# Kernel optimization log

Hardware: AMD Instinct MI355X
Metric: run time of the kernel (lower is better)

The kernel has to match this reference:

```python
import jax, jax.numpy as jnp
import numpy as np

B, L, H, E = 4, 1024, 8, 64
MODES = 64
SCALE = float(1.0 / np.sqrt(512.0))        # 1/sqrt(out_channels)
N_TOP = int(5 * np.ceil(np.log(L)))        # factor * ceil(log(L_Q)) = 35


def setup_inputs() -> dict:
    key = jax.random.key(0)
    k1, k2, k3, k4, k5, k6, k7 = jax.random.split(key, 7)
    rng = np.random.default_rng(0)
    mode_index = jnp.asarray(np.sort(rng.choice(L // 2, MODES, replace=False)), dtype=jnp.int32)
    return {
        "tf_queries": jax.random.normal(k1, (B, L, H, E), dtype=jnp.float32),
        "queries": jax.random.normal(k2, (B, L, H, E), dtype=jnp.float32),
        "keys": jax.random.normal(k3, (B, L, H, E), dtype=jnp.float32),
        "values": jax.random.normal(k4, (B, L, H, E), dtype=jnp.float32),
        "weights1_real": SCALE * jax.random.uniform(k5, (H, E, E, MODES), dtype=jnp.float32),
        "weights1_imag": SCALE * jax.random.uniform(k6, (H, E, E, MODES), dtype=jnp.float32),
        "mix_weights": jax.random.uniform(k7, (H, L, 2), dtype=jnp.float32),
        "mask": jnp.ones((B, L), dtype=jnp.bool_),
        "mode_index": mode_index,
    }


def _sig_scores(q_blhe, k_blhe, corr):
    # q_blhe, k_blhe: [B, L, H, E]
    q = jnp.transpose(q_blhe, (0, 2, 1, 3))  # [B,H,L,E]
    k = jnp.transpose(k_blhe, (0, 2, 1, 3))  # [B,H,L,E]
    if corr:
        # FFT autocorrelation along time
        qf = jnp.fft.rfft(jnp.transpose(q_blhe, (0, 2, 3, 1)), axis=-1)  # [B,H,E,F]
        kf = jnp.fft.rfft(jnp.transpose(k_blhe, (0, 2, 3, 1)), axis=-1)
        ac = jnp.fft.irfft(qf * jnp.conj(kf), n=L, axis=-1)              # [B,H,E,L]
        ac = jnp.transpose(ac, (0, 1, 3, 2))                             # [B,H,L,E]
    else:
        ac = q
    amp = jnp.linalg.norm(ac, axis=-1)                # [B,H,L]
    _, top_idx = jax.lax.top_k(amp, N_TOP)            # [B,H,n]
    q_sel = jnp.take_along_axis(q, top_idx[..., None], axis=2)          # [B,H,n,E]
    scores = jnp.einsum('bhnd,bhmd->bhnm', q_sel, k) * SCALE            # [B,H,n,L]
    full = jnp.full((q.shape[0], H, L, L), -jnp.inf, dtype=q.dtype)
    b_ix = jnp.arange(q.shape[0])[:, None, None]
    h_ix = jnp.arange(H)[None, :, None]
    full = full.at[b_ix, h_ix, top_idx].set(scores)   # scatter selected query rows
    # transpose (L_Q <-> L_K) then softmax over L_Q; -inf rows never occur per-key
    return jax.nn.softmax(jnp.swapaxes(full, 2, 3), axis=-1)            # [B,H,L_K,L_Q]


def reference(tf_queries, queries, keys, values, weights1_real, weights1_imag,
              mix_weights, mask, mode_index):
    attn_t = _sig_scores(queries, keys, corr=True)
    attn_tf = _sig_scores(tf_queries, tf_queries, corr=False)
    nw = jax.nn.softmax(mix_weights, axis=-1)                 # [H,L,2]
    fused = nw[None, :, :, 0, None] * attn_t + nw[None, :, :, 1, None] * attn_tf
    # dropout(p=0.1) is identity in eval mode

    # Fourier mode-mixing branch (computed as in original; its result feeds
    # final_output which the original forward computes but does not return)
    x = jnp.transpose(queries, (0, 2, 3, 1))                  # [B,H,E,L]
    x_ft = jnp.fft.rfft(x, axis=-1)                           # [B,H,E,F]
    W1 = weights1_real + 1j * weights1_imag                   # [H,E,E,MODES]
    x_sel = x_ft[..., mode_index]                             # [B,H,E,MODES]
    out_modes = jnp.einsum('bhim,hiom->bhom', x_sel, W1)      # [B,H,E,MODES]
    out_ft = jnp.zeros(x_ft.shape, dtype=out_modes.dtype).at[..., :MODES].set(out_modes)
    x_mix = jnp.fft.irfft(out_ft, n=L, axis=-1)               # [B,H,E,L]

    output = jnp.einsum('bhlm,bhmd->bhld', fused, jnp.transpose(values, (0, 2, 1, 3)))
    output = jnp.transpose(output, (0, 1, 3, 2))              # [B,H,D,L]
    _final_output = (output + x_mix) / 2                      # unused, as in original
    return output
```

## Files before the change

### kernel.cpp

```cpp
#include <hip/hip_runtime.h>

#define LSEQ 1024
#define NH 8
#define NE 64
#define NTOP 35
#define QKSCALE 0.04419417382415922f

typedef unsigned long long u64;

#define ZP(i) ((i) + ((i) >> 4))

#define FMA4(d, v, sc) \
  (d).x = fmaf((v).x, (sc), (d).x); (d).y = fmaf((v).y, (sc), (d).y); \
  (d).z = fmaf((v).z, (sc), (d).z); (d).w = fmaf((v).w, (sc), (d).w);

__device__ __forceinline__ float2 cadd(float2 a, float2 b) {
  return make_float2(a.x + b.x, a.y + b.y);
}
__device__ __forceinline__ float2 csub(float2 a, float2 b) {
  return make_float2(a.x - b.x, a.y - b.y);
}
__device__ __forceinline__ float2 cmul(float2 a, float2 w) {
  return make_float2(a.x * w.x - a.y * w.y, a.x * w.y + a.y * w.x);
}
__device__ __forceinline__ float2 cmulc(float2 a, float2 w) {
  return make_float2(a.x * w.x + a.y * w.y, a.y * w.x - a.x * w.y);
}
__device__ __forceinline__ void btf4f(float2& x0, float2& x1, float2& x2,
                                      float2& x3, float2 w1, float2 w2,
                                      float2 w3) {
  float2 t0 = cadd(x0, x2), t1 = cadd(x1, x3), t2 = csub(x0, x2);
  float2 d = csub(x1, x3);
  float2 t3 = make_float2(d.y, -d.x);
  x0 = cadd(t0, t1);
  x1 = cmul(cadd(t2, t3), w1);
  x2 = cmul(csub(t0, t1), w2);
  x3 = cmul(csub(t2, t3), w3);
}
__device__ __forceinline__ void btf4i(float2& x0, float2& x1, float2& x2,
                                      float2& x3, float2 w1, float2 w2,
                                      float2 w3) {
  float2 b1 = cmulc(x1, w1), b2 = cmulc(x2, w2), b3 = cmulc(x3, w3);
  float2 A = cadd(x0, b2), B = csub(x0, b2);
  float2 C = cadd(b1, b3), D = csub(b1, b3);
  x0 = cadd(A, C);
  x1 = make_float2(B.x - D.y, B.y + D.x);
  x2 = csub(A, C);
  x3 = make_float2(B.x + D.y, B.y - D.x);
}
__device__ __forceinline__ int rev4(int p) {
  return ((p & 3) << 8) | (((p >> 2) & 3) << 6) | (((p >> 4) & 3) << 4) |
         (((p >> 6) & 3) << 2) | ((p >> 8) & 3);
}

__global__ __launch_bounds__(512) void fft_norm_kernel(
    const float* __restrict__ qm, const float* __restrict__ km,
    const float* __restrict__ tfq,
    float* __restrict__ amp_part, float* __restrict__ norms) {
  const int tid  = threadIdx.x;
  const int hb   = tid >> 8;
  const int ltid = tid & 255;
  const int bh = blockIdx.x & 31;
  const int g4 = blockIdx.x >> 5;
  const int b = bh >> 3, h = bh & 7;

  __shared__ float2 zz[2][2][1088];
  __shared__ float2 tw[1024];

  for (int j = tid; j < 1024; j += 512) {
    float sn, cs;
    sincosf(6.283185307179586f * (float)j * (1.0f / 1024.0f), &sn, &cs);
    tw[j] = make_float2(cs, -sn);
  }

#pragma unroll
  for (int s2 = 0; s2 < 2; ++s2) {
    int slot = tid + (s2 << 9);
    int r = slot >> 4, le = slot & 15;
    int l = (g4 << 6) + r;
    const float* row = tfq + ((size_t)(b * LSEQ + l) * NH + h) * NE;
    float4 v = *(const float4*)(row + (le << 2));
    float s = v.x * v.x + v.y * v.y + v.z * v.z + v.w * v.w;
#pragma unroll
    for (int off = 8; off > 0; off >>= 1) s += __shfl_xor(s, off, 16);
    if (le == 0) norms[(size_t)bh * LSEQ + l] = s;
  }

  const int pair = (g4 << 1) + hb;
  const size_t base =
      (size_t)b * (LSEQ * NH * NE) + (size_t)h * NE + (pair << 1);
  float2* z0 = zz[hb][0];
  float2* z1 = zz[hb][1];

  float2 a0[4], a1[4];
#pragma unroll
  for (int j = 0; j < 4; ++j) {
    int t = ltid + (j << 8);
    float2 qv = *(const float2*)(qm + base + (size_t)t * (NH * NE));
    float2 kv = *(const float2*)(km + base + (size_t)t * (NH * NE));
    a0[j] = make_float2(qv.x, kv.x);
    a1[j] = make_float2(qv.y, kv.y);
  }
  __syncthreads();

  {
    float2 w1 = tw[ltid], w2 = tw[2 * ltid], w3 = tw[3 * ltid];
    btf4f(a0[0], a0[1], a0[2], a0[3], w1, w2, w3);
    btf4f(a1[0], a1[1], a1[2], a1[3], w1, w2, w3);
  }
#pragma unroll
  for (int j = 0; j < 4; ++j) {
    int t = ltid + (j << 8);
    z0[ZP(t)] = a0[j];
    z1[ZP(t)] = a1[j];
  }
  __syncthreads();

#pragma unroll
  for (int st = 0; st < 4; ++st) {
    const int l2h = 6 - 2 * st, l2S = 8 - 2 * st, sc = 2 + 2 * st;
    const int hh = 1 << l2h;
    const int q = ltid & (hh - 1);
    const int idx = ((ltid >> l2h) << l2S) + q;
    const int e1 = q << sc;
    float2 w1 = tw[e1], w2 = tw[2 * e1], w3 = tw[3 * e1];
    int i0 = ZP(idx), i1 = ZP(idx + hh), i2 = ZP(idx + 2 * hh),
        i3 = ZP(idx + 3 * hh);
    float2 x0 = z0[i0], x1 = z0[i1], x2 = z0[i2], x3 = z0[i3];
    btf4f(x0, x1, x2, x3, w1, w2, w3);
    z0[i0] = x0; z0[i1] = x1; z0[i2] = x2; z0[i3] = x3;
    x0 = z1[i0]; x1 = z1[i1]; x2 = z1[i2]; x3 = z1[i3];
    btf4f(x0, x1, x2, x3, w1, w2, w3);
    z1[i0] = x0; z1[i1] = x1; z1[i2] = x2; z1[i3] = x3;
    __syncthreads();
  }

  float2 yv[4];
#pragma unroll
  for (int j = 0; j < 4; ++j) {
    int p = ltid + (j << 8);
    int f = rev4(p);
    int fm = (1024 - f) & 1023;
    int pm = rev4(fm);
    float2 A0 = z0[ZP(p)], B0 = z0[ZP(pm)];
    float2 A1 = z1[ZP(p)], B1 = z1[ZP(pm)];
    float2 Q0 = make_float2(0.5f * (A0.x + B0.x), 0.5f * (A0.y - B0.y));
    float2 iK0 = make_float2(0.5f * (A0.x - B0.x), 0.5f * (A0.y + B0.y));
    float2 K0 = make_float2(iK0.y, -iK0.x);
    float2 P0 = make_float2(Q0.x * K0.x + Q0.y * K0.y,
                            Q0.y * K0.x - Q0.x * K0.y);
    float2 Q1 = make_float2(0.5f * (A1.x + B1.x), 0.5f * (A1.y - B1.y));
    float2 iK1 = make_float2(0.5f * (A1.x - B1.x), 0.5f * (A1.y + B1.y));
    float2 K1 = make_float2(iK1.y, -iK1.x);
    float2 P1 = make_float2(Q1.x * K1.x + Q1.y * K1.y,
                            Q1.y * K1.x - Q1.x * K1.y);
    yv[j] = make_float2(P0.x - P1.y, P0.y + P1.x);
  }
  __syncthreads();
#pragma unroll
  for (int j = 0; j < 4; ++j) z0[ZP(ltid + (j << 8))] = yv[j];
  __syncthreads();

#pragma unroll
  for (int st = 0; st < 4; ++st) {
    const int l2h = 2 * st, l2S = 2 * st + 2, sc = 8 - 2 * st;
    const int hh = 1 << l2h;
    const int q = ltid & (hh - 1);
    const int idx = ((ltid >> l2h) << l2S) + q;
    const int e1 = q << sc;
    float2 w1 = tw[e1], w2 = tw[2 * e1], w3 = tw[3 * e1];
    int i0 = ZP(idx), i1 = ZP(idx + hh), i2 = ZP(idx + 2 * hh),
        i3 = ZP(idx + 3 * hh);
    float2 x0 = z0[i0], x1 = z0[i1], x2 = z0[i2], x3 = z0[i3];
    btf4i(x0, x1, x2, x3, w1, w2, w3);
    z0[i0] = x0; z0[i1] = x1; z0[i2] = x2; z0[i3] = x3;
    __syncthreads();
  }

#pragma unroll
  for (int j = 0; j < 4; ++j) a0[j] = z0[ZP(ltid + (j << 8))];
  {
    float2 w1 = tw[ltid], w2 = tw[2 * ltid], w3 = tw[3 * ltid];
    btf4i(a0[0], a0[1], a0[2], a0[3], w1, w2, w3);
  }
  const float inv = 1.0f / 1024.0f;
  float* pp = amp_part + ((size_t)pair * 32 + bh) * LSEQ;
#pragma unroll
  for (int j = 0; j < 4; ++j) {
    int t = ltid + (j << 8);
    float2 y = a0[j];
    pp[t] = (y.x * y.x + y.y * y.y) * inv * inv;
  }
}

__global__ __launch_bounds__(256) void topk_kernel(
    const float* __restrict__ amp_part, const float* __restrict__ norms,
    int* __restrict__ sel_t, int* __restrict__ sel_tf) {
  __shared__ int hist[256];
  __shared__ int sufarr[256];
  __shared__ int wtot[4];
  __shared__ int sh_d, sh_r;
  __shared__ int wcnt[4][4];

  const int tid = threadIdx.x;
  const int bh = blockIdx.x & 31;
  const int arr = blockIdx.x >> 5;
  int* sel = (arr == 0 ? sel_t : sel_tf) + bh * NTOP;
  const int wave = tid >> 6, lane = tid & 63;

  u64 key[4];
  if (arr == 0) {
    float a[4] = {0.f, 0.f, 0.f, 0.f};
    for (int p = 0; p < 32; ++p) {
      const float* pp = amp_part + ((size_t)p * 32 + bh) * LSEQ + tid;
#pragma unroll
      for (int j = 0; j < 4; ++j) a[j] += pp[j << 8];
    }
#pragma unroll
    for (int j = 0; j < 4; ++j) {
      int l = tid + (j << 8);
      key[j] = ((u64)__float_as_uint(a[j]) << 32) | (unsigned)(LSEQ - 1 - l);
    }
  } else {
    const float* sc = norms + (size_t)bh * LSEQ;
#pragma unroll
    for (int j = 0; j < 4; ++j) {
      int l = tid + (j << 8);
      key[j] = ((u64)__float_as_uint(sc[l]) << 32) | (unsigned)(LSEQ - 1 - l);
    }
  }

  u64 prefix = 0, pmask = 0;
  int r = NTOP;
  const int shifts[6] = {56, 48, 40, 32, 8, 0};
#pragma unroll
  for (int pass = 0; pass < 6; ++pass) {
    const int sh = shifts[pass];
    hist[tid] = 0;
    __syncthreads();
#pragma unroll
    for (int j = 0; j < 4; ++j)
      if ((key[j] & pmask) == prefix)
        atomicAdd(&hist[(int)((key[j] >> sh) & 255)], 1);
    __syncthreads();
    int v = hist[tid];
#pragma unroll
    for (int off = 1; off < 64; off <<= 1) {
      int o = __shfl_down(v, (unsigned)off);
      if (lane + off < 64) v += o;
    }
    if (lane == 0) wtot[wave] = v;
    __syncthreads();
    int add = 0;
    for (int w = wave + 1; w < 4; ++w) add += wtot[w];
    sufarr[tid] = v + add;
    __syncthreads();
    int suf = sufarr[tid];
    int sufn = (tid < 255) ? sufarr[tid + 1] : 0;
    if (suf >= r && sufn < r) { sh_d = tid; sh_r = r - sufn; }
    __syncthreads();
    prefix |= ((u64)sh_d) << sh;
    pmask  |= ((u64)255) << sh;
    r = sh_r;
    __syncthreads();
  }
  const u64 T = prefix;

  u64 bmask[4];
#pragma unroll
  for (int j = 0; j < 4; ++j) {
    bmask[j] = __ballot(key[j] >= T);
    if (lane == 0) wcnt[j][wave] = __popcll(bmask[j]);
  }
  __syncthreads();
#pragma unroll
  for (int j = 0; j < 4; ++j) {
    if (key[j] >= T) {
      int lim = (j << 2) + wave;
      int base = 0;
      for (int idx = 0; idx < lim; ++idx) base += wcnt[idx >> 2][idx & 3];
      int pos = base + __popcll(bmask[j] & ((1ull << lane) - 1ull));
      sel[pos] = tid + (j << 8);
    }
  }
}

__global__ __launch_bounds__(512) void attn_out_kernel(
    const float* __restrict__ qm, const float* __restrict__ tfq,
    const float* __restrict__ km, const float* __restrict__ vm,
    const float* __restrict__ mixw,
    const int* __restrict__ sel_t, const int* __restrict__ sel_tf,
    float* __restrict__ out) {
  __shared__ float Qs[2 * 40 * 68];
  __shared__ float Xs[2 * 64 * 132];
  __shared__ float Ss[2 * 40 * 132];
  __shared__ float Vs[2 * 36 * 68];

  const int tid = threadIdx.x;
  const int kc = blockIdx.x & 7;
  const int bh = blockIdx.x >> 3;
  const int b = bh >> 3, h = bh & 7;
  const int k0 = kc << 7;
  const size_t base = (size_t)b * (LSEQ * NH * NE) + (size_t)h * NE;

  for (int i = tid; i < 1280; i += 512) {
    int r = i >> 4, e4 = (i & 15) << 2;
    int br = (r >= 40), n = r - (br ? 40 : 0);
    float4 v = make_float4(0.f, 0.f, 0.f, 0.f);
    if (n < NTOP) {
      int l = (br ? sel_tf : sel_t)[bh * NTOP + n];
      v = *(const float4*)((br ? tfq : qm) + base + (size_t)l * (NH * NE) + e4);
    }
    *(float4*)&Qs[r * 68 + e4] = v;
  }
  for (int i = tid; i < 1152; i += 512) {
    int r = i >> 4, e4 = (i & 15) << 2;
    int br = (r >= 36), n = r - (br ? 36 : 0);
    float4 v = make_float4(0.f, 0.f, 0.f, 0.f);
    if (n < NTOP) {
      int l = (br ? sel_tf : sel_t)[bh * NTOP + n];
      v = *(const float4*)(vm + base + (size_t)l * (NH * NE) + e4);
    }
    *(float4*)&Vs[r * 68 + e4] = v;
  }
  for (int i = tid; i < 4096; i += 512) {
    int br = i >> 11, k = (i >> 4) & 127, e4 = (i & 15) << 2;
    const float* xsrc = br ? tfq : km;
    float4 v = *(const float4*)(xsrc + base + (size_t)(k0 + k) * (NH * NE) + e4);
    float* X = Xs + br * (64 * 132);
    X[(e4 + 0) * 132 + k] = v.x;
    X[(e4 + 1) * 132 + k] = v.y;
    X[(e4 + 2) * 132 + k] = v.z;
    X[(e4 + 3) * 132 + k] = v.w;
  }
  __syncthreads();

  {
    const int s = tid >> 5;
    const int kq4 = (tid & 31) << 2;
    const float* Xb = Xs + (s >> 3) * (64 * 132);
    float4 acc[5];
#pragma unroll
    for (int r = 0; r < 5; ++r) acc[r] = make_float4(0.f, 0.f, 0.f, 0.f);
    for (int e0 = 0; e0 < NE; e0 += 4) {
      float4 xv0 = *(const float4*)&Xb[(e0 + 0) * 132 + kq4];
      float4 xv1 = *(const float4*)&Xb[(e0 + 1) * 132 + kq4];
      float4 xv2 = *(const float4*)&Xb[(e0 + 2) * 132 + kq4];
      float4 xv3 = *(const float4*)&Xb[(e0 + 3) * 132 + kq4];
#pragma unroll
      for (int r = 0; r < 5; ++r) {
        float4 qv = *(const float4*)&Qs[(s * 5 + r) * 68 + e0];
        FMA4(acc[r], xv0, qv.x);
        FMA4(acc[r], xv1, qv.y);
        FMA4(acc[r], xv2, qv.z);
        FMA4(acc[r], xv3, qv.w);
      }
    }
#pragma unroll
    for (int r = 0; r < 5; ++r)
      *(float4*)&Ss[(s * 5 + r) * 132 + kq4] = acc[r];
  }
  __syncthreads();

  if (tid < 256) {
    const int k = tid & 127, br = tid >> 7;
    float p[NTOP];
    float mx = -1e30f;
#pragma unroll
    for (int n = 0; n < NTOP; ++n) {
      p[n] = Ss[(br * 40 + n) * 132 + k] * QKSCALE;
      mx = fmaxf(mx, p[n]);
    }
    float sum = 0.f;
#pragma unroll
    for (int n = 0; n < NTOP; ++n) { p[n] = __expf(p[n] - mx); sum += p[n]; }
    const float w0 = mixw[(size_t)h * (LSEQ * 2) + (size_t)(k0 + k) * 2 + 0];
    const float w1 = mixw[(size_t)h * (LSEQ * 2) + (size_t)(k0 + k) * 2 + 1];
    const float ew0 = __expf(w0), ew1 = __expf(w1);
    const float c = (br ? ew1 : ew0) / ((ew0 + ew1) * sum);
#pragma unroll
    for (int n = 0; n < NTOP; ++n) Ss[(br * 40 + n) * 132 + k] = p[n] * c;
  }
  __syncthreads();

  {
    const int kq4 = (tid & 31) << 2;
    const int d0 = (tid >> 5) << 2;
    float4 a[4];
#pragma unroll
    for (int dj = 0; dj < 4; ++dj) a[dj] = make_float4(0.f, 0.f, 0.f, 0.f);
#pragma unroll 5
    for (int n = 0; n < NTOP; ++n) {
      float4 p0 = *(const float4*)&Ss[n * 132 + kq4];
      float4 vv = *(const float4*)&Vs[n * 68 + d0];
      FMA4(a[0], p0, vv.x);
      FMA4(a[1], p0, vv.y);
      FMA4(a[2], p0, vv.z);
      FMA4(a[3], p0, vv.w);
    }
#pragma unroll 5
    for (int n = 0; n < NTOP; ++n) {
      float4 p1 = *(const float4*)&Ss[(40 + n) * 132 + kq4];
      float4 vv = *(const float4*)&Vs[(36 + n) * 68 + d0];
      FMA4(a[0], p1, vv.x);
      FMA4(a[1], p1, vv.y);
      FMA4(a[2], p1, vv.z);
      FMA4(a[3], p1, vv.w);
    }
    float* ob = out + (size_t)bh * (NE * LSEQ) + k0 + kq4;
#pragma unroll
    for (int dj = 0; dj < 4; ++dj)
      *(float4*)&ob[(size_t)(d0 + dj) * LSEQ] = a[dj];
  }
}

extern "C" void kernel_launch(void* const* d_in, const int* in_sizes, int n_in,
                              void* d_out, int out_size, void* d_ws, size_t ws_size,
                              hipStream_t stream) {
  const float* tfq  = (const float*)d_in[0];
  const float* qm   = (const float*)d_in[1];
  const float* km   = (const float*)d_in[2];
  const float* vm   = (const float*)d_in[3];
  const float* mixw = (const float*)d_in[6];

  float* amp_part = (float*)d_ws;
  float* norms    = amp_part + 32 * 32 * LSEQ;
  int*   sel_t    = (int*)(norms + 32 * LSEQ);
  int*   sel_tf   = sel_t + 32 * NTOP;
  float* out      = (float*)d_out;

  fft_norm_kernel<<<dim3(512), dim3(512), 0, stream>>>(qm, km, tfq,
                                                       amp_part, norms);
  topk_kernel<<<dim3(64), dim3(256), 0, stream>>>(amp_part, norms,
                                                  sel_t, sel_tf);
  attn_out_kernel<<<dim3(256), dim3(512), 0, stream>>>(qm, tfq, km, vm, mixw,
                                                       sel_t, sel_tf, out);
}
```

Measured before the change: 52.01 us.

## Pre-gather selected Q/V rows in top-k kernel and halve attention key tile

The top-k kernel now keeps the selected indices in shared memory and writes packed, zero-padded Q and V rows to a workspace. The attention kernel then loads these rows contiguously instead of doing the indirect gathers itself. The attention grid doubles to 512 blocks with 64-key tiles. The score buffer now reuses the transposed-X shared buffer, which cuts shared memory and should raise occupancy. The cost is extra global traffic for the packed buffers, extra serial work in the 64-block top-k kernel, and half as much work per thread using float2 instead of float4 operations.

After: 51.75 us, median of 2. No clear change (-0.5%).

```diff
diff --git a/kernel.cpp b/kernel.cpp
--- a/kernel.cpp
+++ b/kernel.cpp
@@ -10,9 +10,8 @@
 
 #define ZP(i) ((i) + ((i) >> 4))
 
-#define FMA4(d, v, sc) \
-  (d).x = fmaf((v).x, (sc), (d).x); (d).y = fmaf((v).y, (sc), (d).y); \
-  (d).z = fmaf((v).z, (sc), (d).z); (d).w = fmaf((v).w, (sc), (d).w);
+#define FMA2(d, v, sc) \
+  (d).x = fmaf((v).x, (sc), (d).x); (d).y = fmaf((v).y, (sc), (d).y);
 
 __device__ __forceinline__ float2 cadd(float2 a, float2 b) {
   return make_float2(a.x + b.x, a.y + b.y);
@@ -193,19 +192,22 @@
   }
 }
 
-__global__ __launch_bounds__(256) void topk_kernel(
+__global__ __launch_bounds__(256) void topk_pack_kernel(
     const float* __restrict__ amp_part, const float* __restrict__ norms,
-    int* __restrict__ sel_t, int* __restrict__ sel_tf) {
+    const float* __restrict__ qm, const float* __restrict__ tfq,
+    const float* __restrict__ vm,
+    float* __restrict__ Qp, float* __restrict__ Vp) {
   __shared__ int hist[256];
   __shared__ int sufarr[256];
   __shared__ int wtot[4];
   __shared__ int sh_d, sh_r;
   __shared__ int wcnt[4][4];
+  __shared__ int selsh[NTOP];
 
   const int tid = threadIdx.x;
   const int bh = blockIdx.x & 31;
   const int arr = blockIdx.x >> 5;
-  int* sel = (arr == 0 ? sel_t : sel_tf) + bh * NTOP;
+  const int b = bh >> 3, h = bh & 7;
   const int wave = tid >> 6, lane = tid & 63;
 
   u64 key[4];
@@ -277,98 +279,106 @@
   for (int j = 0; j < 4; ++j) {
     if (key[j] >= T) {
       int lim = (j << 2) + wave;
-      int base = 0;
-      for (int idx = 0; idx < lim; ++idx) base += wcnt[idx >> 2][idx & 3];
-      int pos = base + __popcll(bmask[j] & ((1ull << lane) - 1ull));
-      sel[pos] = tid + (j << 8);
-    }
+      int base2 = 0;
+      for (int idx = 0; idx < lim; ++idx) base2 += wcnt[idx >> 2][idx & 3];
+      int pos = base2 + __popcll(bmask[j] & ((1ull << lane) - 1ull));
+      selsh[pos] = tid + (j << 8);
+    }
+  }
+  __syncthreads();
+
+  const size_t base = (size_t)b * (LSEQ * NH * NE) + (size_t)h * NE;
+  const float* qsrc = arr ? tfq : qm;
+  float* qdst = Qp + ((size_t)(bh * 2 + arr) * 40) * NE;
+  for (int i = tid; i < 640; i += 256) {
+    int rr = i >> 4, e4 = (i & 15) << 2;
+    float4 v = make_float4(0.f, 0.f, 0.f, 0.f);
+    if (rr < NTOP)
+      v = *(const float4*)(qsrc + base + (size_t)selsh[rr] * (NH * NE) + e4);
+    *(float4*)(qdst + rr * NE + e4) = v;
+  }
+  float* vdst = Vp + ((size_t)(bh * 2 + arr) * 36) * NE;
+  for (int i = tid; i < 576; i += 256) {
+    int rr = i >> 4, e4 = (i & 15) << 2;
+    float4 v = make_float4(0.f, 0.f, 0.f, 0.f);
+    if (rr < NTOP)
+      v = *(const float4*)(vm + base + (size_t)selsh[rr] * (NH * NE) + e4);
+    *(float4*)(vdst + rr * NE + e4) = v;
   }
 }
 
 __global__ __launch_bounds__(512) void attn_out_kernel(
-    const float* __restrict__ qm, const float* __restrict__ tfq,
-    const float* __restrict__ km, const float* __restrict__ vm,
-    const float* __restrict__ mixw,
-    const int* __restrict__ sel_t, const int* __restrict__ sel_tf,
-    float* __restrict__ out) {
-  __shared__ float Qs[2 * 40 * 68];
-  __shared__ float Xs[2 * 64 * 132];
-  __shared__ float Ss[2 * 40 * 132];
-  __shared__ float Vs[2 * 36 * 68];
+    const float* __restrict__ tfq, const float* __restrict__ km,
+    const float* __restrict__ Qp, const float* __restrict__ Vp,
+    const float* __restrict__ mixw, float* __restrict__ out) {
+  __shared__ float Qs[80 * 68];
+  __shared__ float XSs[2 * 64 * 68];
+  __shared__ float Vs[72 * 68];
 
   const int tid = threadIdx.x;
-  const int kc = blockIdx.x & 7;
-  const int bh = blockIdx.x >> 3;
+  const int kc = blockIdx.x & 15;
+  const int bh = blockIdx.x >> 4;
   const int b = bh >> 3, h = bh & 7;
-  const int k0 = kc << 7;
+  const int k0 = kc << 6;
   const size_t base = (size_t)b * (LSEQ * NH * NE) + (size_t)h * NE;
 
   for (int i = tid; i < 1280; i += 512) {
-    int r = i >> 4, e4 = (i & 15) << 2;
-    int br = (r >= 40), n = r - (br ? 40 : 0);
-    float4 v = make_float4(0.f, 0.f, 0.f, 0.f);
-    if (n < NTOP) {
-      int l = (br ? sel_tf : sel_t)[bh * NTOP + n];
-      v = *(const float4*)((br ? tfq : qm) + base + (size_t)l * (NH * NE) + e4);
-    }
-    *(float4*)&Qs[r * 68 + e4] = v;
+    int rr = i >> 4, e4 = (i & 15) << 2;
+    *(float4*)&Qs[rr * 68 + e4] =
+        *(const float4*)(Qp + ((size_t)bh * 80 + rr) * NE + e4);
   }
   for (int i = tid; i < 1152; i += 512) {
-    int r = i >> 4, e4 = (i & 15) << 2;
-    int br = (r >= 36), n = r - (br ? 36 : 0);
-    float4 v = make_float4(0.f, 0.f, 0.f, 0.f);
-    if (n < NTOP) {
-      int l = (br ? sel_tf : sel_t)[bh * NTOP + n];
-      v = *(const float4*)(vm + base + (size_t)l * (NH * NE) + e4);
-    }
-    *(float4*)&Vs[r * 68 + e4] = v;
-  }
-  for (int i = tid; i < 4096; i += 512) {
-    int br = i >> 11, k = (i >> 4) & 127, e4 = (i & 15) << 2;
+    int rr = i >> 4, e4 = (i & 15) << 2;
+    *(float4*)&Vs[rr * 68 + e4] =
+        *(const float4*)(Vp + ((size_t)bh * 72 + rr) * NE + e4);
+  }
+  for (int i = tid; i < 2048; i += 512) {
+    int br = i >> 10, k = (i >> 4) & 63, e4 = (i & 15) << 2;
     const float* xsrc = br ? tfq : km;
     float4 v = *(const float4*)(xsrc + base + (size_t)(k0 + k) * (NH * NE) + e4);
-    float* X = Xs + br * (64 * 132);
-    X[(e4 + 0) * 132 + k] = v.x;
-    X[(e4 + 1) * 132 + k] = v.y;
-    X[(e4 + 2) * 132 + k] = v.z;
-    X[(e4 + 3) * 132 + k] = v.w;
-  }
-  __syncthreads();
-
+    float* X = XSs + br * (64 * 68);
+    X[(e4 + 0) * 68 + k] = v.x;
+    X[(e4 + 1) * 68 + k] = v.y;
+    X[(e4 + 2) * 68 + k] = v.z;
+    X[(e4 + 3) * 68 + k] = v.w;
+  }
+  __syncthreads();
+
+  const int s = tid >> 5;
+  const int kq2 = (tid & 31) << 1;
+  float2 acc[5];
   {
-    const int s = tid >> 5;
-    const int kq4 = (tid & 31) << 2;
-    const float* Xb = Xs + (s >> 3) * (64 * 132);
-    float4 acc[5];
-#pragma unroll
-    for (int r = 0; r < 5; ++r) acc[r] = make_float4(0.f, 0.f, 0.f, 0.f);
+    const float* Xb = XSs + (s >> 3) * (64 * 68);
+#pragma unroll
+    for (int r = 0; r < 5; ++r) acc[r] = make_float2(0.f, 0.f);
     for (int e0 = 0; e0 < NE; e0 += 4) {
-      float4 xv0 = *(const float4*)&Xb[(e0 + 0) * 132 + kq4];
-      float4 xv1 = *(const float4*)&Xb[(e0 + 1) * 132 + kq4];
-      float4 xv2 = *(const float4*)&Xb[(e0 + 2) * 132 + kq4];
-      float4 xv3 = *(const float4*)&Xb[(e0 + 3) * 132 + kq4];
+      float2 xv0 = *(const float2*)&Xb[(e0 + 0) * 68 + kq2];
+      float2 xv1 = *(const float2*)&Xb[(e0 + 1) * 68 + kq2];
+      float2 xv2 = *(const float2*)&Xb[(e0 + 2) * 68 + kq2];
+      float2 xv3 = *(const float2*)&Xb[(e0 + 3) * 68 + kq2];
 #pragma unroll
       for (int r = 0; r < 5; ++r) {
         float4 qv = *(const float4*)&Qs[(s * 5 + r) * 68 + e0];
-        FMA4(acc[r], xv0, qv.x);
-        FMA4(acc[r], xv1, qv.y);
-        FMA4(acc[r], xv2, qv.z);
-        FMA4(acc[r], xv3, qv.w);
+        FMA2(acc[r], xv0, qv.x);
+        FMA2(acc[r], xv1, qv.y);
+        FMA2(acc[r], xv2, qv.z);
+        FMA2(acc[r], xv3, qv.w);
       }
     }
-#pragma unroll
-    for (int r = 0; r < 5; ++r)
-      *(float4*)&Ss[(s * 5 + r) * 132 + kq4] = acc[r];
-  }
-  __syncthreads();
-
-  if (tid < 256) {
-    const int k = tid & 127, br = tid >> 7;
+  }
+  __syncthreads();
+#pragma unroll
+  for (int r = 0; r < 5; ++r)
+    *(float2*)&XSs[(s * 5 + r) * 68 + kq2] = acc[r];
+  __syncthreads();
+
+  if (tid < 128) {
+    const int k = tid & 63, br = tid >> 6;
     float p[NTOP];
     float mx = -1e30f;
 #pragma unroll
     for (int n = 0; n < NTOP; ++n) {
-      p[n] = Ss[(br * 40 + n) * 132 + k] * QKSCALE;
+      p[n] = XSs[(br * 40 + n) * 68 + k] * QKSCALE;
       mx = fmaxf(mx, p[n]);
     }
     float sum = 0.f;
@@ -379,38 +389,37 @@
     const float ew0 = __expf(w0), ew1 = __expf(w1);
     const float c = (br ? ew1 : ew0) / ((ew0 + ew1) * sum);
 #pragma unroll
-    for (int n = 0; n < NTOP; ++n) Ss[(br * 40 + n) * 132 + k] = p[n] * c;
+    for (int n = 0; n < NTOP; ++n) XSs[(br * 40 + n) * 68 + k] = p[n] * c;
   }
   __syncthreads();
 
   {
-    const int kq4 = (tid & 31) << 2;
     const int d0 = (tid >> 5) << 2;
-    float4 a[4];
-#pragma unroll
-    for (int dj = 0; dj < 4; ++dj) a[dj] = make_float4(0.f, 0.f, 0.f, 0.f);
+    float2 a[4];
+#pragma unroll
+    for (int dj = 0; dj < 4; ++dj) a[dj] = make_float2(0.f, 0.f);
 #pragma unroll 5
     for (int n = 0; n < NTOP; ++n) {
-      float4 p0 = *(const float4*)&Ss[n * 132 + kq4];
+      float2 p0 = *(const float2*)&XSs[n * 68 + kq2];
       float4 vv = *(const float4*)&Vs[n * 68 + d0];
-      FMA4(a[0], p0, vv.x);
-      FMA4(a[1], p0, vv.y);
-      FMA4(a[2], p0, vv.z);
-      FMA4(a[3], p0, vv.w);
+      FMA2(a[0], p0, vv.x);
+      FMA2(a[1], p0, vv.y);
+      FMA2(a[2], p0, vv.z);
+      FMA2(a[3], p0, vv.w);
     }
 #pragma unroll 5
     for (int n = 0; n < NTOP; ++n) {
-      float4 p1 = *(const float4*)&Ss[(40 + n) * 132 + kq4];
+      float2 p1 = *(const float2*)&XSs[(40 + n) * 68 + kq2];
       float4 vv = *(const float4*)&Vs[(36 + n) * 68 + d0];
-      FMA4(a[0], p1, vv.x);
-      FMA4(a[1], p1, vv.y);
-      FMA4(a[2], p1, vv.z);
-      FMA4(a[3], p1, vv.w);
-    }
-    float* ob = out + (size_t)bh * (NE * LSEQ) + k0 + kq4;
+      FMA2(a[0], p1, vv.x);
+      FMA2(a[1], p1, vv.y);
+      FMA2(a[2], p1, vv.z);
+      FMA2(a[3], p1, vv.w);
+    }
+    float* ob = out + (size_t)bh * (NE * LSEQ) + k0 + kq2;
 #pragma unroll
     for (int dj = 0; dj < 4; ++dj)
-      *(float4*)&ob[(size_t)(d0 + dj) * LSEQ] = a[dj];
+      *(float2*)&ob[(size_t)(d0 + dj) * LSEQ] = a[dj];
   }
 }
 
@@ -425,14 +434,14 @@
 
   float* amp_part = (float*)d_ws;
   float* norms    = amp_part + 32 * 32 * LSEQ;
-  int*   sel_t    = (int*)(norms + 32 * LSEQ);
-  int*   sel_tf   = sel_t + 32 * NTOP;
+  float* Qp       = norms + 32 * LSEQ;
+  float* Vp       = Qp + 32 * 80 * NE;
   float* out      = (float*)d_out;
 
   fft_norm_kernel<<<dim3(512), dim3(512), 0, stream>>>(qm, km, tfq,
                                                        amp_part, norms);
-  topk_kernel<<<dim3(64), dim3(256), 0, stream>>>(amp_part, norms,
-                                                  sel_t, sel_tf);
-  attn_out_kernel<<<dim3(256), dim3(512), 0, stream>>>(qm, tfq, km, vm, mixw,
-                                                       sel_t, sel_tf, out);
-}
+  topk_pack_kernel<<<dim3(64), dim3(256), 0, stream>>>(amp_part, norms,
+                                                       qm, tfq, vm, Qp, Vp);
+  attn_out_kernel<<<dim3(512), dim3(512), 0, stream>>>(tfq, km, Qp, Vp,
+                                                       mixw, out);
+}
```
